# Performance work log

Measured on AMD Instinct MI355X. Metric: run time of the kernel, lower is better.

## Reference

```python
import jax, jax.numpy as jnp
import numpy as np

B, S, D = 2, 2048, 1024
H, DA, DL = 8, 64, 64   # heads, attention_dim, linear_dim
L = 2                    # num_blocks


def _layernorm(x, w, b, eps):
    mu = jnp.mean(x, axis=-1, keepdims=True)
    var = jnp.mean(jnp.square(x - mu), axis=-1, keepdims=True)
    return (x - mu) * jax.lax.rsqrt(var + eps) * w + b


def _norm_no_affine(x, eps):
    mu = jnp.mean(x, axis=-1, keepdims=True)
    var = jnp.mean(jnp.square(x - mu), axis=-1, keepdims=True)
    return (x - mu) * jax.lax.rsqrt(var + eps)


def setup_inputs() -> dict:
    key = jax.random.key(0)
    ks = jax.random.split(key, 8)
    x = jax.random.normal(ks[0], (B, S, D), dtype=jnp.float32)
    # causal visibility mask: True = visible
    attn_mask = jnp.tril(jnp.ones((S, S), dtype=bool))[None].repeat(B, axis=0)
    proj_dim = DL * 2 * H + DA * 2 * H  # 2048
    uvqk = jax.random.normal(ks[1], (L, D, proj_dim), dtype=jnp.float32) * 0.02
    o_w = jax.random.normal(ks[2], (L, D, DL * H), dtype=jnp.float32) * 0.02  # torch [out,in]
    o_b = jnp.zeros((L, D), dtype=jnp.float32)
    ln_w = jnp.ones((L, D), dtype=jnp.float32)
    ln_b = jnp.zeros((L, D), dtype=jnp.float32)
    last_ln_w = jnp.ones((D,), dtype=jnp.float32)
    last_ln_b = jnp.zeros((D,), dtype=jnp.float32)
    return {"x": x, "attn_mask": attn_mask, "uvqk": uvqk, "o_w": o_w,
            "o_b": o_b, "ln_w": ln_w, "ln_b": ln_b,
            "last_ln_w": last_ln_w, "last_ln_b": last_ln_b}


def reference(x, attn_mask, uvqk, o_w, o_b, ln_w, ln_b, last_ln_w, last_ln_b):
    seq_len = x.shape[1]
    m = attn_mask[:, None, :, :]  # [B,1,S,S]
    for i in range(L):
        h = _layernorm(x, ln_w[i], ln_b[i], 1e-6)                 # [B,S,D]
        proj = jax.nn.silu(jnp.einsum('bsd,de->bse', h, uvqk[i]))  # [B,S,2*(DL+DA)*H]
        u, v, q, k = jnp.split(proj, [DL * H, 2 * DL * H, 2 * DL * H + DA * H], axis=-1)
        q = q.reshape(B, seq_len, H, DA).transpose(0, 2, 1, 3)   # [B,H,S,DA]
        kk = k.reshape(B, seq_len, H, DA).transpose(0, 2, 1, 3)
        vv = v.reshape(B, seq_len, H, DL).transpose(0, 2, 1, 3)  # [B,H,S,DL]
        uu = u.reshape(B, seq_len, H, DL).transpose(0, 2, 1, 3)
        scores = jnp.einsum('bhsd,bhtd->bhst', q, kk)            # [B,H,S,S]
        scores = jnp.where(m, jax.nn.silu(scores) / seq_len, 0.0)
        out = jnp.einsum('bhst,bhtd->bhsd', scores, vv)          # [B,H,S,DL]
        out = _norm_no_affine(out, 1e-6)
        u_dot = (uu * out).transpose(0, 2, 1, 3).reshape(B, seq_len, DL * H)
        x = x + jnp.einsum('bsf,df->bsd', u_dot, o_w[i]) + o_b[i]
    return _layernorm(x, last_ln_w, last_ln_b, 1e-8)
```

## Files before the change

kernel.cpp:

```cpp
#include <hip/hip_runtime.h>

#define B_ 2
#define S_ 2048
#define D_ 1024
#define H_ 8
#define L_ 2
#define P_ 2048
#define F_ 512
#define R_ (B_*S_)

typedef unsigned short u16;
typedef unsigned int u32;
typedef __bf16 bf16;
typedef bf16 bf16x8 __attribute__((ext_vector_type(8)));
typedef short short8 __attribute__((ext_vector_type(8)));
typedef float v4f __attribute__((ext_vector_type(4)));

__device__ __forceinline__ float silu_fast(float x){
  float e = __expf(-x);
  return x * __builtin_amdgcn_rcpf(1.0f + e);
}
__device__ __forceinline__ float bf2f(u16 u){
  union { u32 i; float f; } x; x.i = ((u32)u) << 16; return x.f;
}
__device__ __forceinline__ u16 f2bfu(float f){
  union { float f; u32 i; } x; x.f = f;
  u32 r = x.i + 0x7fff + ((x.i >> 16) & 1);
  return (u16)(r >> 16);
}
__device__ __forceinline__ void gload16(const u16* g, u16* l){
  __builtin_amdgcn_global_load_lds(
      (const __attribute__((address_space(1))) void*)g,
      (__attribute__((address_space(3))) void*)l, 16, 0, 0);
}

__global__ __launch_bounds__(256) void cvt_kernel(const float* __restrict__ x, float* __restrict__ xf){
  int i = (blockIdx.x * 256 + threadIdx.x) * 4;
  *(float4*)(xf + i) = *(const float4*)(x + i);
}

__global__ __launch_bounds__(256) void cvt_bf16_kernel(const float* __restrict__ src, u16* __restrict__ dst){
  int i = (blockIdx.x * 256 + threadIdx.x) * 4;
  float4 v = *(const float4*)(src + i);
  ushort4 o; o.x = f2bfu(v.x); o.y = f2bfu(v.y); o.z = f2bfu(v.z); o.w = f2bfu(v.w);
  *(ushort4*)(dst + i) = o;
}

__global__ __launch_bounds__(256) void cvt_uvqkT_kernel(const float* __restrict__ uvqk, u16* __restrict__ ot){
  __shared__ float t[32][33];
  int l = blockIdx.z;
  int p0 = blockIdx.x * 32, d0 = blockIdx.y * 32;
  int tx = threadIdx.x & 31, ty = threadIdx.x >> 5;
  const float* src = uvqk + ((size_t)l * D_ + d0) * P_ + p0;
  #pragma unroll
  for (int s = 0; s < 4; s++)
    t[ty + s*8][tx] = src[(size_t)(ty + s*8) * P_ + tx];
  __syncthreads();
  u16* dst = ot + ((size_t)l * P_ + p0) * D_ + d0;
  #pragma unroll
  for (int s = 0; s < 4; s++)
    dst[(size_t)(ty + s*8) * D_ + tx] = f2bfu(t[tx][ty + s*8]);
}

__global__ __launch_bounds__(256) void kvpack_kernel(const u16* __restrict__ projh,
    u16* __restrict__ kpack, u16* __restrict__ vpack, float* __restrict__ opart){
  __shared__ u16 tls[64*72];
  int t = blockIdx.x, t0 = t * 64;
  int bh = blockIdx.y;
  int b = bh >> 3, hh = bh & 7;
  int tid = threadIdx.x;
  const size_t bS = (size_t)b * S_;
  const int voff = F_ + hh*64, koff = 3*F_ + hh*64;
  {
    float* zp = opart + (size_t)(bh*32 + t) * 4096 + tid * 16;
    #pragma unroll
    for (int i = 0; i < 4; i++)
      *(float4*)(zp + i*4) = make_float4(0.f, 0.f, 0.f, 0.f);
  }
  {
    int row = tid >> 2, c16 = (tid & 3) * 16;
    const u16* sp = projh + (bS + t0 + row) * P_ + voff + c16;
    short8 a = *(const short8*)sp;
    short8 bq = *(const short8*)(sp + 8);
    *(short8*)&tls[row*72 + c16] = a;
    *(short8*)&tls[row*72 + c16 + 8] = bq;
  }
  __syncthreads();
  size_t obase = ((size_t)(bh*32 + t) * 8) * 512;
  #pragma unroll
  for (int pass = 0; pass < 2; pass++){
    int id = tid + pass * 256;
    int c = id >> 6, lane = id & 63;
    int quad = lane >> 4, l15 = lane & 15;
    int cns = c >> 1, ckst = c & 1;
    const u16* kp = projh + (bS + t0 + cns*16 + l15) * P_ + koff + ckst*32 + quad*8;
    *(short8*)(kpack + obase + (size_t)c*512 + lane*8) = *(const short8*)kp;
    short8 vv;
    #pragma unroll
    for (int j = 0; j < 8; j++)
      vv[j] = (short)tls[(ckst*32 + quad*8 + j)*72 + cns*16 + l15];
    *(short8*)(vpack + obase + (size_t)c*512 + lane*8) = vv;
  }
}

__global__ __launch_bounds__(256) void ln_kernel(const float* __restrict__ xf,
    const float* __restrict__ w, const float* __restrict__ b,
    void* __restrict__ outp, float eps, int out_bf16){
  int row = blockIdx.x, tid = threadIdx.x;
  const float* xr = xf + (size_t)row * D_;
  float4 v = *(const float4*)(xr + tid * 4);
  float s  = v.x + v.y + v.z + v.w;
  float sq = v.x*v.x + v.y*v.y + v.z*v.z + v.w*v.w;
  #pragma unroll
  for (int off = 32; off; off >>= 1){ s += __shfl_down(s, off); sq += __shfl_down(sq, off); }
  __shared__ float red[8];
  __shared__ float stats[2];
  int wid = tid >> 6;
  if ((tid & 63) == 0){ red[wid] = s; red[4 + wid] = sq; }
  __syncthreads();
  if (tid == 0){
    float S1 = red[0] + red[1] + red[2] + red[3];
    float S2 = red[4] + red[5] + red[6] + red[7];
    float mu = S1 * (1.0f / D_);
    float var = S2 * (1.0f / D_) - mu * mu;
    stats[0] = mu; stats[1] = rsqrtf(var + eps);
  }
  __syncthreads();
  float mu = stats[0], rs = stats[1];
  int i = tid * 4;
  float4 wv = *(const float4*)(w + i);
  float4 bv = *(const float4*)(b + i);
  float o0 = (v.x - mu) * rs * wv.x + bv.x;
  float o1 = (v.y - mu) * rs * wv.y + bv.y;
  float o2 = (v.z - mu) * rs * wv.z + bv.z;
  float o3 = (v.w - mu) * rs * wv.w + bv.w;
  if (out_bf16){
    ushort4 o; o.x = f2bfu(o0); o.y = f2bfu(o1); o.z = f2bfu(o2); o.w = f2bfu(o3);
    *(ushort4*)((u16*)outp + (size_t)row * D_ + i) = o;
  } else {
    *(float4*)((float*)outp + (size_t)row * D_ + i) = make_float4(o0, o1, o2, o3);
  }
}

template<int KDIM>
__device__ __forceinline__ void gemm_mfma_core(const u16* __restrict__ A,
    const u16* __restrict__ Bt, u16* As, u16* Bs, int m0, int n0, v4f acc[4][4]){
  int tid = threadIdx.x;
  int w = tid >> 6, lane = tid & 63;
  int wm = w >> 1, wn = w & 1, quad = lane >> 4, l15 = lane & 15;
  int srow = lane >> 2, skoct = (lane & 3) * 8;
  for (int kt = 0; kt < KDIM; kt += 32){
    __syncthreads();
    #pragma unroll
    for (int s = 0; s < 2; s++){
      int g = w * 2 + s;
      gload16(A  + (size_t)(m0 + g*16 + srow) * KDIM + kt + skoct, As + g*512);
      gload16(Bt + (size_t)(n0 + g*16 + srow) * KDIM + kt + skoct, Bs + g*512);
    }
    __syncthreads();
    short8 af[4], bfr[4];
    #pragma unroll
    for (int i = 0; i < 4; i++)
      af[i] = *(const short8*)&As[(wm*64 + i*16 + l15)*32 + quad*8];
    #pragma unroll
    for (int j = 0; j < 4; j++)
      bfr[j] = *(const short8*)&Bs[(wn*64 + j*16 + l15)*32 + quad*8];
    #pragma unroll
    for (int i = 0; i < 4; i++)
      #pragma unroll
      for (int j = 0; j < 4; j++)
        acc[i][j] = __builtin_amdgcn_mfma_f32_16x16x32_bf16(
            __builtin_bit_cast(bf16x8, af[i]), __builtin_bit_cast(bf16x8, bfr[j]),
            acc[i][j], 0, 0, 0);
  }
}

__global__ __launch_bounds__(256) void gemm_silu_mfma(const u16* __restrict__ A,
    const u16* __restrict__ Bt, u16* __restrict__ C){
  __shared__ u16 As[128*32], Bs[128*32];
  v4f acc[4][4];
  #pragma unroll
  for (int i = 0; i < 4; i++)
    #pragma unroll
    for (int j = 0; j < 4; j++) acc[i][j] = (v4f){0.f,0.f,0.f,0.f};
  int m0 = blockIdx.y * 128, n0 = blockIdx.x * 128;
  gemm_mfma_core<D_>(A, Bt, As, Bs, m0, n0, acc);
  int tid = threadIdx.x, w = tid >> 6, lane = tid & 63;
  int wm = w >> 1, wn = w & 1, quad = lane >> 4, l15 = lane & 15;
  #pragma unroll
  for (int i = 0; i < 4; i++)
    #pragma unroll
    for (int r = 0; r < 4; r++){
      int m = m0 + wm*64 + i*16 + quad*4 + r;
      u16* cp = C + (size_t)m * P_ + n0 + wn*64 + l15;
      #pragma unroll
      for (int j = 0; j < 4; j++)
        cp[j*16] = f2bfu(silu_fast(acc[i][j][r]));
    }
}

__global__ __launch_bounds__(256) void gemm_add_mfma(const u16* __restrict__ A,
    const u16* __restrict__ Bt, const float* __restrict__ bias, float* __restrict__ X){
  __shared__ u16 As[128*32], Bs[128*32];
  v4f acc[4][4];
  #pragma unroll
  for (int i = 0; i < 4; i++)
    #pragma unroll
    for (int j = 0; j < 4; j++) acc[i][j] = (v4f){0.f,0.f,0.f,0.f};
  int m0 = blockIdx.y * 128, n0 = blockIdx.x * 128;
  gemm_mfma_core<F_>(A, Bt, As, Bs, m0, n0, acc);
  int tid = threadIdx.x, w = tid >> 6, lane = tid & 63;
  int wm = w >> 1, wn = w & 1, quad = lane >> 4, l15 = lane & 15;
  float bj[4];
  #pragma unroll
  for (int j = 0; j < 4; j++) bj[j] = bias[n0 + wn*64 + j*16 + l15];
  #pragma unroll
  for (int i = 0; i < 4; i++)
    #pragma unroll
    for (int r = 0; r < 4; r++){
      int m = m0 + wm*64 + i*16 + quad*4 + r;
      float* xp = X + (size_t)m * D_ + n0 + wn*64 + l15;
      #pragma unroll
      for (int j = 0; j < 4; j++)
        xp[j*16] += acc[i][j][r] + bj[j];
    }
}

__global__ __launch_bounds__(256) void attn_kernel(const u16* __restrict__ projh,
                                                   const u16* __restrict__ kpack,
                                                   const u16* __restrict__ vpack,
                                                   float* __restrict__ opart){
  __shared__ u16 ks[8*512];
  __shared__ u16 vs[8*512];
  __shared__ u16 Ps[64*72];
  int qt = 15 - (int)blockIdx.x;
  int z  = blockIdx.z;
  int ttop = 2*qt + 1;
  if (z > ttop) return;
  int bh = blockIdx.y;
  int b = bh >> 3, hh = bh & 7;
  int tid = threadIdx.x;
  int w = tid >> 6, lane = tid & 63, quad = lane >> 4, l15 = lane & 15;
  int s0 = qt * 128;
  const size_t bS = (size_t)b * S_;
  const int qoff = 2*F_ + hh*64;

  bf16x8 aq[2][2];
  #pragma unroll
  for (int qh = 0; qh < 2; qh++){
    const u16* qp = projh + (bS + s0 + qh*64 + w*16 + l15) * P_ + qoff + quad*8;
    aq[qh][0] = __builtin_bit_cast(bf16x8, *(const short8*)qp);
    aq[qh][1] = __builtin_bit_cast(bf16x8, *(const short8*)(qp + 32));
  }

  v4f oacc[2][4];
  #pragma unroll
  for (int qh = 0; qh < 2; qh++)
    #pragma unroll
    for (int i = 0; i < 4; i++) oacc[qh][i] = (v4f){0.f, 0.f, 0.f, 0.f};

  for (int t = z; t <= ttop; t += 4){
    size_t pbase = ((size_t)(bh*32 + t) * 8) * 512;
    __syncthreads();
    #pragma unroll
    for (int cc = 0; cc < 2; cc++){
      int c = w + cc*4;
      gload16(kpack + pbase + (size_t)c*512 + lane*8, ks + c*512);
      gload16(vpack + pbase + (size_t)c*512 + lane*8, vs + c*512);
    }
    __syncthreads();

    short8 vf[4][2];
    #pragma unroll
    for (int ds = 0; ds < 4; ds++)
      #pragma unroll
      for (int kst = 0; kst < 2; kst++)
        vf[ds][kst] = *(const short8*)&vs[(ds*2+kst)*512 + lane*8];

    int t0 = t * 64;
    #pragma unroll
    for (int qh = 0; qh < 2; qh++){
      int dtile = 2*qt + qh;
      if (t > dtile) continue;
      v4f sacc[4];
      #pragma unroll
      for (int i = 0; i < 4; i++) sacc[i] = (v4f){0.f, 0.f, 0.f, 0.f};
      #pragma unroll
      for (int ns = 0; ns < 4; ns++){
        bf16x8 bk0 = __builtin_bit_cast(bf16x8, *(const short8*)&ks[(ns*2+0)*512 + lane*8]);
        bf16x8 bk1 = __builtin_bit_cast(bf16x8, *(const short8*)&ks[(ns*2+1)*512 + lane*8]);
        sacc[ns] = __builtin_amdgcn_mfma_f32_16x16x32_bf16(aq[qh][0], bk0, sacc[ns], 0, 0, 0);
        sacc[ns] = __builtin_amdgcn_mfma_f32_16x16x32_bf16(aq[qh][1], bk1, sacc[ns], 0, 0, 0);
      }

      bool diag = (t == dtile);
      #pragma unroll
      for (int ns = 0; ns < 4; ns++){
        #pragma unroll
        for (int r = 0; r < 4; r++){
          int rl = w*16 + quad*4 + r;
          int cl = ns*16 + l15;
          float p = silu_fast(sacc[ns][r]) * (1.0f / S_);
          if (diag && cl > rl) p = 0.0f;
          Ps[rl*72 + cl] = f2bfu(p);
        }
      }
      #pragma unroll
      for (int kst = 0; kst < 2; kst++){
        short8 aps = *(const short8*)&Ps[(w*16 + l15)*72 + kst*32 + quad*8];
        bf16x8 ap = __builtin_bit_cast(bf16x8, aps);
        #pragma unroll
        for (int ds = 0; ds < 4; ds++)
          oacc[qh][ds] = __builtin_amdgcn_mfma_f32_16x16x32_bf16(
              ap, __builtin_bit_cast(bf16x8, vf[ds][kst]), oacc[qh][ds], 0, 0, 0);
      }
    }
  }

  #pragma unroll
  for (int qh = 0; qh < 2; qh++){
    if (z > 2*qt + qh) continue;
    #pragma unroll
    for (int r = 0; r < 4; r++){
      int sg = s0 + qh*64 + w*16 + quad*4 + r;
      float* op = opart + (bS + sg) * (size_t)F_ + hh*64 + l15;
      #pragma unroll
      for (int ds = 0; ds < 4; ds++)
        atomicAdd(op + ds*16, oacc[qh][ds][r]);
    }
  }
}

__global__ __launch_bounds__(256) void norm_gate_kernel(const float* __restrict__ opart,
    const u16* __restrict__ projh, u16* __restrict__ udot){
  int w = threadIdx.x >> 6, lane = threadIdx.x & 63;
  int sg = blockIdx.x * 4 + w;
  int hh = lane >> 3, seg = lane & 7;
  const float* op = opart + (size_t)sg * F_ + hh*64 + seg*8;
  v4f e0 = *(const v4f*)op;
  v4f e1 = *(const v4f*)(op + 4);
  float s  = e0[0]+e0[1]+e0[2]+e0[3] + e1[0]+e1[1]+e1[2]+e1[3];
  float sq = e0[0]*e0[0]+e0[1]*e0[1]+e0[2]*e0[2]+e0[3]*e0[3]
           + e1[0]*e1[0]+e1[1]*e1[1]+e1[2]*e1[2]+e1[3]*e1[3];
  #pragma unroll
  for (int m = 1; m < 8; m <<= 1){
    s  += __shfl_xor(s, m, 64);
    sq += __shfl_xor(sq, m, 64);
  }
  float mu = s * (1.0f/64.0f);
  float var = sq * (1.0f/64.0f) - mu*mu;
  float rs = rsqrtf(var + 1e-6f);
  const u16* up = projh + (size_t)sg * P_ + hh*64 + seg*8;
  short8 uv = *(const short8*)up;
  short8 ov;
  #pragma unroll
  for (int e = 0; e < 4; e++)
    ov[e] = (short)f2bfu((e0[e] - mu) * rs * bf2f((u16)uv[e]));
  #pragma unroll
  for (int e = 0; e < 4; e++)
    ov[4+e] = (short)f2bfu((e1[e] - mu) * rs * bf2f((u16)uv[4+e]));
  *(short8*)(udot + (size_t)sg * F_ + hh*64 + seg*8) = ov;
}

extern "C" void kernel_launch(void* const* d_in, const int* in_sizes, int n_in,
                              void* d_out, int out_size, void* d_ws, size_t ws_size,
                              hipStream_t stream){
  (void)in_sizes; (void)n_in; (void)out_size; (void)ws_size;
  const float* x     = (const float*)d_in[0];
  const float* uvqk  = (const float*)d_in[2];
  const float* o_w   = (const float*)d_in[3];
  const float* o_b   = (const float*)d_in[4];
  const float* ln_w  = (const float*)d_in[5];
  const float* ln_b  = (const float*)d_in[6];
  const float* lln_w = (const float*)d_in[7];
  const float* lln_b = (const float*)d_in[8];
  float* out = (float*)d_out;

  char* ws = (char*)d_ws;
  float* xf    = (float*)ws;
  u16*   h     = (u16*)(ws + (16u<<20));
  u16*   kpack = h;
  u16*   vpack = (u16*)(ws + (20u<<20));
  u16*   udot  = (u16*)(ws + (24u<<20));
  u16*   projh = (u16*)(ws + (28u<<20));
  u16*   uvqkT = (u16*)(ws + (44u<<20));
  u16*   owh   = (u16*)(ws + (52u<<20));
  float* opart = (float*)(ws + (54u<<20));

  cvt_kernel<<<R_ * D_ / 1024, 256, 0, stream>>>(x, xf);
  cvt_uvqkT_kernel<<<dim3(P_/32, D_/32, L_), 256, 0, stream>>>(uvqk, uvqkT);
  cvt_bf16_kernel<<<L_ * D_ * F_ / 1024, 256, 0, stream>>>(o_w, owh);
  for (int l = 0; l < L_; l++){
    ln_kernel<<<R_, 256, 0, stream>>>(xf, ln_w + l * D_, ln_b + l * D_, h, 1e-6f, 1);
    gemm_silu_mfma<<<dim3(P_/128, R_/128), 256, 0, stream>>>(
        h, uvqkT + (size_t)l * P_ * D_, projh);
    kvpack_kernel<<<dim3(S_/64, B_*H_), 256, 0, stream>>>(projh, kpack, vpack, opart);
    attn_kernel<<<dim3(S_/128, B_*H_, 4), 256, 0, stream>>>(projh, kpack, vpack, opart);
    norm_gate_kernel<<<R_/4, 256, 0, stream>>>(opart, projh, udot);
    gemm_add_mfma<<<dim3(D_/128, R_/128), 256, 0, stream>>>(
        udot, owh + (size_t)l * D_ * F_, o_b + l * D_, xf);
  }
  ln_kernel<<<R_, 256, 0, stream>>>(xf, lln_w, lln_b, out, 1e-8f, 0);
}
```

Measured before the change: 325.8 us.

## Replace atomic split-K attention reduction with two bf16 partial buffers

The attention kernel's KV split is cut from four ways to two. Each split now writes its partial output to its own bf16 buffer with plain stores instead of doing fp32 atomicAdd into a zeroed buffer. The norm_gate kernel sums the two partials on load, and the zeroing in kvpack is removed. This drops atomic traffic and the memset, and halves the partial-buffer bytes. In exchange there is less parallelism per query tile and some extra rounding, since partials are stored in bf16 before the sum.

```diff
diff --git a/kernel.cpp b/kernel.cpp
--- a/kernel.cpp
+++ b/kernel.cpp
@@ -63,7 +63,7 @@
 }
 
 __global__ __launch_bounds__(256) void kvpack_kernel(const u16* __restrict__ projh,
-    u16* __restrict__ kpack, u16* __restrict__ vpack, float* __restrict__ opart){
+    u16* __restrict__ kpack, u16* __restrict__ vpack){
   __shared__ u16 tls[64*72];
   int t = blockIdx.x, t0 = t * 64;
   int bh = blockIdx.y;
@@ -71,12 +71,6 @@
   int tid = threadIdx.x;
   const size_t bS = (size_t)b * S_;
   const int voff = F_ + hh*64, koff = 3*F_ + hh*64;
-  {
-    float* zp = opart + (size_t)(bh*32 + t) * 4096 + tid * 16;
-    #pragma unroll
-    for (int i = 0; i < 4; i++)
-      *(float4*)(zp + i*4) = make_float4(0.f, 0.f, 0.f, 0.f);
-  }
   {
     int row = tid >> 2, c16 = (tid & 3) * 16;
     const u16* sp = projh + (bS + t0 + row) * P_ + voff + c16;
@@ -229,14 +223,13 @@
 __global__ __launch_bounds__(256) void attn_kernel(const u16* __restrict__ projh,
                                                    const u16* __restrict__ kpack,
                                                    const u16* __restrict__ vpack,
-                                                   float* __restrict__ opart){
+                                                   u16* __restrict__ opart){
   __shared__ u16 ks[8*512];
   __shared__ u16 vs[8*512];
   __shared__ u16 Ps[64*72];
   int qt = 15 - (int)blockIdx.x;
   int z  = blockIdx.z;
   int ttop = 2*qt + 1;
-  if (z > ttop) return;
   int bh = blockIdx.y;
   int b = bh >> 3, hh = bh & 7;
   int tid = threadIdx.x;
@@ -259,7 +252,7 @@
     #pragma unroll
     for (int i = 0; i < 4; i++) oacc[qh][i] = (v4f){0.f, 0.f, 0.f, 0.f};
 
-  for (int t = z; t <= ttop; t += 4){
+  for (int t = z; t <= ttop; t += 2){
     size_t pbase = ((size_t)(bh*32 + t) * 8) * 512;
     __syncthreads();
     #pragma unroll
@@ -317,31 +310,35 @@
     }
   }
 
+  u16* ob = opart + (size_t)z * ((size_t)R_ * F_);
   #pragma unroll
   for (int qh = 0; qh < 2; qh++){
-    if (z > 2*qt + qh) continue;
     #pragma unroll
     for (int r = 0; r < 4; r++){
       int sg = s0 + qh*64 + w*16 + quad*4 + r;
-      float* op = opart + (bS + sg) * (size_t)F_ + hh*64 + l15;
+      u16* op = ob + (bS + sg) * (size_t)F_ + hh*64 + l15;
       #pragma unroll
       for (int ds = 0; ds < 4; ds++)
-        atomicAdd(op + ds*16, oacc[qh][ds][r]);
-    }
-  }
-}
-
-__global__ __launch_bounds__(256) void norm_gate_kernel(const float* __restrict__ opart,
+        op[ds*16] = f2bfu(oacc[qh][ds][r]);
+    }
+  }
+}
+
+__global__ __launch_bounds__(256) void norm_gate_kernel(const u16* __restrict__ opart,
     const u16* __restrict__ projh, u16* __restrict__ udot){
   int w = threadIdx.x >> 6, lane = threadIdx.x & 63;
   int sg = blockIdx.x * 4 + w;
   int hh = lane >> 3, seg = lane & 7;
-  const float* op = opart + (size_t)sg * F_ + hh*64 + seg*8;
-  v4f e0 = *(const v4f*)op;
-  v4f e1 = *(const v4f*)(op + 4);
-  float s  = e0[0]+e0[1]+e0[2]+e0[3] + e1[0]+e1[1]+e1[2]+e1[3];
-  float sq = e0[0]*e0[0]+e0[1]*e0[1]+e0[2]*e0[2]+e0[3]*e0[3]
-           + e1[0]*e1[0]+e1[1]*e1[1]+e1[2]*e1[2]+e1[3]*e1[3];
+  size_t off = (size_t)sg * F_ + hh*64 + seg*8;
+  short8 a0 = *(const short8*)(opart + off);
+  short8 a1 = *(const short8*)(opart + (size_t)R_ * F_ + off);
+  float e[8];
+  float s = 0.f, sq = 0.f;
+  #pragma unroll
+  for (int i = 0; i < 8; i++){
+    e[i] = bf2f((u16)a0[i]) + bf2f((u16)a1[i]);
+    s += e[i]; sq += e[i]*e[i];
+  }
   #pragma unroll
   for (int m = 1; m < 8; m <<= 1){
     s  += __shfl_xor(s, m, 64);
@@ -354,12 +351,9 @@
   short8 uv = *(const short8*)up;
   short8 ov;
   #pragma unroll
-  for (int e = 0; e < 4; e++)
-    ov[e] = (short)f2bfu((e0[e] - mu) * rs * bf2f((u16)uv[e]));
-  #pragma unroll
-  for (int e = 0; e < 4; e++)
-    ov[4+e] = (short)f2bfu((e1[e] - mu) * rs * bf2f((u16)uv[4+e]));
-  *(short8*)(udot + (size_t)sg * F_ + hh*64 + seg*8) = ov;
+  for (int i = 0; i < 8; i++)
+    ov[i] = (short)f2bfu((e[i] - mu) * rs * bf2f((u16)uv[i]));
+  *(short8*)(udot + off) = ov;
 }
 
 extern "C" void kernel_launch(void* const* d_in, const int* in_sizes, int n_in,
@@ -385,7 +379,7 @@
   u16*   projh = (u16*)(ws + (28u<<20));
   u16*   uvqkT = (u16*)(ws + (44u<<20));
   u16*   owh   = (u16*)(ws + (52u<<20));
-  float* opart = (float*)(ws + (54u<<20));
+  u16*   opart = (u16*)(ws + (54u<<20));
 
   cvt_kernel<<<R_ * D_ / 1024, 256, 0, stream>>>(x, xf);
   cvt_uvqkT_kernel<<<dim3(P_/32, D_/32, L_), 256, 0, stream>>>(uvqk, uvqkT);
@@ -394,8 +388,8 @@
     ln_kernel<<<R_, 256, 0, stream>>>(xf, ln_w + l * D_, ln_b + l * D_, h, 1e-6f, 1);
     gemm_silu_mfma<<<dim3(P_/128, R_/128), 256, 0, stream>>>(
         h, uvqkT + (size_t)l * P_ * D_, projh);
-    kvpack_kernel<<<dim3(S_/64, B_*H_), 256, 0, stream>>>(projh, kpack, vpack, opart);
-    attn_kernel<<<dim3(S_/128, B_*H_, 4), 256, 0, stream>>>(projh, kpack, vpack, opart);
+    kvpack_kernel<<<dim3(S_/64, B_*H_), 256, 0, stream>>>(projh, kpack, vpack);
+    attn_kernel<<<dim3(S_/128, B_*H_, 2), 256, 0, stream>>>(projh, kpack, vpack, opart);
     norm_gate_kernel<<<R_/4, 256, 0, stream>>>(opart, projh, udot);
     gemm_add_mfma<<<dim3(D_/128, R_/128), 256, 0, stream>>>(
         udot, owh + (size_t)l * D_ * F_, o_b + l * D_, xf);
```

Result: no change. 325.6 us (-0.1%).
